# Optimization experiments

Hardware: AMD Instinct MI355X
Metric: run time of the kernel (lower is better)

The kernel has to match this reference:

```python
import jax, jax.numpy as jnp
import numpy as np

B, S, D = 2, 2048, 2048
H, DH = 16, 128


def _rope(x, position):
    # x: [B, H, S, DH], position: [B, S]
    dh = x.shape[-1]
    inv_freq = 1.0 / (10000.0 ** (jnp.arange(0, dh, 2, dtype=jnp.float32) / dh))
    freqs = position.astype(jnp.float32)[:, :, None] * inv_freq[None, None, :]  # [B, S, DH/2]
    emb = jnp.concatenate([freqs, freqs], axis=-1)  # [B, S, DH]
    cos = jnp.cos(emb)[:, None, :, :]
    sin = jnp.sin(emb)[:, None, :, :]
    x1, x2 = x[..., : dh // 2], x[..., dh // 2 :]
    rot = jnp.concatenate([-x2, x1], axis=-1)
    return x * cos + rot * sin


def setup_inputs() -> dict:
    key = jax.random.key(0)
    ks = jax.random.split(key, 5)
    hidden_state = jax.random.normal(ks[0], (B, S, D), dtype=jnp.float32)
    mask = jnp.broadcast_to(jnp.tril(jnp.ones((S, S), dtype=bool)), (B, S, S))
    position = jnp.broadcast_to(jnp.arange(S, dtype=jnp.int64), (B, S))
    scale = 1.0 / np.sqrt(D)
    Wq = jax.random.normal(ks[1], (D, H * DH), dtype=jnp.float32) * scale
    Wk = jax.random.normal(ks[2], (D, H * DH), dtype=jnp.float32) * scale
    Wv = jax.random.normal(ks[3], (D, H * DH), dtype=jnp.float32) * scale
    Wo = jax.random.normal(ks[4], (H * DH, D), dtype=jnp.float32) * scale
    return {"hidden_state": hidden_state, "mask": mask, "position": position,
            "Wq": Wq, "Wk": Wk, "Wv": Wv, "Wo": Wo}


def reference(hidden_state, mask, position, Wq, Wk, Wv, Wo):
    b, s, _ = hidden_state.shape
    def split_heads(h):
        return h.reshape(b, s, H, DH).transpose(0, 2, 1, 3)  # [B, H, S, DH]
    h_q = _rope(split_heads(hidden_state @ Wq), position)
    h_k = _rope(split_heads(hidden_state @ Wk), position)
    h_v = split_heads(hidden_state @ Wv)
    score = jnp.einsum('bhqd,bhkd->bhqk', h_q, h_k) / np.sqrt(DH)
    m = mask[:, None, :, :]
    score = jnp.where(m, score, jnp.float32(-jnp.inf))
    probs = jax.nn.softmax(score, axis=-1)
    probs = jnp.where(m, probs, jnp.float32(0.0))
    out = jnp.einsum('bhqk,bhkd->bhqd', probs, h_v)
    out = out.transpose(0, 2, 1, 3).reshape(b, s, H * DH)
    return out @ Wo
```

## Files before the change

### kernel.cpp

```cpp
#include <hip/hip_runtime.h>
#include <hip/hip_bf16.h>

typedef unsigned short u16;
typedef __bf16 bf16x8 __attribute__((ext_vector_type(8)));
typedef float f32x4 __attribute__((ext_vector_type(4)));
typedef unsigned short u16x8 __attribute__((ext_vector_type(8)));

__device__ __forceinline__ u16 f2bf(float f) {
  union { float f; unsigned u; } v; v.f = f;
  unsigned r = (v.u + 0x7FFFu + ((v.u >> 16) & 1u)) >> 16;
  return (u16)r;
}
__device__ __forceinline__ float bf2f(u16 s) {
  union { unsigned u; float f; } v; v.u = ((unsigned)s) << 16;
  return v.f;
}
__device__ __forceinline__ f32x4 zero4() { f32x4 z = {0.f, 0.f, 0.f, 0.f}; return z; }

__device__ __forceinline__ void async16(void* lds, const void* g) {
  __builtin_amdgcn_global_load_lds(
      (__attribute__((address_space(1))) void*)(void*)g,
      (__attribute__((address_space(3))) void*)lds, 16, 0, 0);
}

__global__ void sniff_dtype(const unsigned* __restrict__ X, int* __restrict__ flag) {
  __shared__ int cnt;
  if (threadIdx.x == 0) cnt = 0;
  __syncthreads();
  unsigned w = X[(size_t)threadIdx.x * 16384 + 1000];
  int e = (int)((w >> 7) & 0xFF);
  if (e >= 100 && e <= 150) atomicAdd(&cnt, 1);
  __syncthreads();
  if (threadIdx.x == 0) flag[0] = (cnt < 192) ? 1 : 0;
}

__global__ __launch_bounds__(256) void convert_x(
    const void* __restrict__ X, u16* __restrict__ dst, const int* __restrict__ flag) {
  const int mode = flag[0];
  size_t i8 = ((size_t)blockIdx.x * 256 + threadIdx.x) * 8;
  if (mode) {
    const float4* f = (const float4*)X;
    float4 a = f[i8 / 4], b = f[i8 / 4 + 1];
    u16x8 o;
    o[0] = f2bf(a.x); o[1] = f2bf(a.y); o[2] = f2bf(a.z); o[3] = f2bf(a.w);
    o[4] = f2bf(b.x); o[5] = f2bf(b.y); o[6] = f2bf(b.z); o[7] = f2bf(b.w);
    *(u16x8*)&dst[i8] = o;
  } else {
    *(u16x8*)&dst[i8] = *(const u16x8*)&((const u16*)X)[i8];
  }
}

__global__ __launch_bounds__(256) void transpose_w(
    const void* __restrict__ src, u16* __restrict__ d, const int* __restrict__ flag)
{
  __shared__ u16 t[64][65];
  const int mode = flag[0];
  int r0 = blockIdx.y * 64, c0 = blockIdx.x * 64;
  int tid = threadIdx.x;
  for (int j = 0; j < 2; ++j) {
    int idx = tid + j * 256;
    int r = idx >> 3, c = (idx & 7) * 8;
    size_t base = (size_t)(r0 + r) * 2048 + c0 + c;
    if (mode) {
      const float4* f = (const float4*)src;
      float4 a = f[base / 4], b = f[base / 4 + 1];
      t[r][c + 0] = f2bf(a.x); t[r][c + 1] = f2bf(a.y);
      t[r][c + 2] = f2bf(a.z); t[r][c + 3] = f2bf(a.w);
      t[r][c + 4] = f2bf(b.x); t[r][c + 5] = f2bf(b.y);
      t[r][c + 6] = f2bf(b.z); t[r][c + 7] = f2bf(b.w);
    } else {
      u16x8 v = *(const u16x8*)&((const u16*)src)[base];
      for (int q = 0; q < 8; ++q) t[r][c + q] = v[q];
    }
  }
  __syncthreads();
  for (int j = 0; j < 2; ++j) {
    int idx = tid + j * 256;
    int c = idx >> 3, r = (idx & 7) * 8;
    u16x8 v;
    for (int q = 0; q < 8; ++q) v[q] = t[r + q][c];
    *(u16x8*)&d[(size_t)(c0 + c) * 2048 + r0 + r] = v;
  }
}

__global__ __launch_bounds__(256) void transpose_v(
    const u16* __restrict__ V, u16* __restrict__ Vt)
{
  __shared__ u16 t[64][65];
  int bh = blockIdx.z;
  int b = bh >> 4, h = bh & 15;
  int kv0 = blockIdx.x * 64, d0 = blockIdx.y * 64;
  int tid = threadIdx.x;
  for (int j = 0; j < 2; ++j) {
    int idx = tid + j * 256;
    int r = idx >> 3, c = (idx & 7) * 8;
    u16x8 v = *(const u16x8*)&V[(size_t)(b * 2048 + kv0 + r) * 2048 + h * 128 + d0 + c];
    for (int q = 0; q < 8; ++q) t[r][c + q] = v[q];
  }
  __syncthreads();
  for (int j = 0; j < 2; ++j) {
    int idx = tid + j * 256;
    int c = idx >> 3, r = (idx & 7) * 8;
    u16x8 v;
    for (int q = 0; q < 8; ++q) v[q] = t[r + q][c];
    *(u16x8*)&Vt[((size_t)bh * 128 + d0 + c) * 2048 + kv0 + r] = v;
  }
}

__global__ __launch_bounds__(256) void rope_k(u16* __restrict__ Qp, u16* __restrict__ Kp)
{
  int idx = blockIdx.x * 256 + threadIdx.x;
  u16* X = blockIdx.y ? Kp : Qp;
  int i8 = (idx & 7) * 8;
  int h = (idx >> 3) & 15;
  int tok = idx >> 7;
  int pos = tok & 2047;
  size_t base = (size_t)tok * 2048 + h * 128 + i8;
  u16x8 a = *(const u16x8*)&X[base];
  u16x8 bv = *(const u16x8*)&X[base + 64];
  u16x8 ra, rb;
  for (int j = 0; j < 8; ++j) {
    float fi = (float)(i8 + j);
    float invf = __expf(fi * -0.14391156831212787f);
    float th = (float)pos * invf;
    float c, s;
    sincosf(th, &s, &c);
    float x1 = bf2f(a[j]), x2 = bf2f(bv[j]);
    ra[j] = f2bf(x1 * c - x2 * s);
    rb[j] = f2bf(x2 * c + x1 * s);
  }
  *(u16x8*)&X[base] = ra;
  *(u16x8*)&X[base + 64] = rb;
}

__global__ __launch_bounds__(256) void qkv_gemm(
    const u16* __restrict__ A, const u16* __restrict__ Bt,
    u16* __restrict__ Qw, u16* __restrict__ Kw, u16* __restrict__ Vw)
{
  __shared__ __align__(16) u16 As[128 * 32];
  __shared__ __align__(16) u16 Bs[128 * 32];
  const int K = 2048, N = 2048;
  const int tid = threadIdx.x;
  const int wave = tid >> 6, lane = tid & 63;
  const int quad = lane >> 4, l = lane & 15;
  const int wr = wave >> 1, wc = wave & 1;
  const int m0 = blockIdx.y * 128, n0full = blockIdx.x * 128;
  const int mat = n0full >> 11;
  const int n0 = n0full & 2047;
  u16* C = (mat == 0) ? Qw : ((mat == 1) ? Kw : Vw);

  f32x4 acc[4][4];
  for (int i = 0; i < 4; ++i)
    for (int j = 0; j < 4; ++j) acc[i][j] = zero4();

  int rowA[2], gA[2];
  for (int j = 0; j < 2; ++j) {
    int tf = tid + j * 256;
    rowA[j] = tf >> 2;
    gA[j] = (tf & 3) ^ ((rowA[j] >> 1) & 3);
  }

  for (int kt = 0; kt < K; kt += 32) {
    __syncthreads();
    for (int j = 0; j < 2; ++j) {
      int tf = tid + j * 256;
      async16(&As[tf * 8], &A[(size_t)(m0 + rowA[j]) * K + kt + gA[j] * 8]);
      async16(&Bs[tf * 8], &Bt[(size_t)(n0full + rowA[j]) * K + kt + gA[j] * 8]);
    }
    __syncthreads();

    bf16x8 af[4], bfr[4];
    for (int mt = 0; mt < 4; ++mt) {
      int row = wr * 64 + mt * 16 + l;
      int g = quad ^ ((row >> 1) & 3);
      af[mt] = *(const bf16x8*)&As[row * 32 + g * 8];
    }
    for (int nt = 0; nt < 4; ++nt) {
      int row = wc * 64 + nt * 16 + l;
      int g = quad ^ ((row >> 1) & 3);
      bfr[nt] = *(const bf16x8*)&Bs[row * 32 + g * 8];
    }
    for (int mt = 0; mt < 4; ++mt)
      for (int nt = 0; nt < 4; ++nt)
        acc[mt][nt] = __builtin_amdgcn_mfma_f32_16x16x32_bf16(af[mt], bfr[nt], acc[mt][nt], 0, 0, 0);
  }
  for (int mt = 0; mt < 4; ++mt)
    for (int nt = 0; nt < 4; ++nt)
      for (int r = 0; r < 4; ++r) {
        int m = m0 + wr * 64 + mt * 16 + quad * 4 + r;
        int n = n0 + wc * 64 + nt * 16 + l;
        C[(size_t)m * N + n] = f2bf(acc[mt][nt][r]);
      }
}

__global__ __launch_bounds__(256) void gemm64_bt(
    const u16* __restrict__ A, const u16* __restrict__ Bt, void* __restrict__ C,
    int M, int N, int K, const int* __restrict__ flag, int dual)
{
  __shared__ __align__(16) u16 As[64 * 32];
  __shared__ __align__(16) u16 Bs[64 * 32];
  const int mode = dual ? flag[0] : 0;
  const int tid = threadIdx.x;
  const int wave = tid >> 6, lane = tid & 63;
  const int quad = lane >> 4, l = lane & 15;
  const int wr = wave >> 1, wc = wave & 1;
  const int m0 = blockIdx.y * 64, n0 = blockIdx.x * 64;

  f32x4 acc[2][2];
  for (int i = 0; i < 2; ++i)
    for (int j = 0; j < 2; ++j) acc[i][j] = zero4();

  const int rowA = tid >> 2;
  const int gA = (tid & 3) ^ ((rowA >> 1) & 3);

  for (int kt = 0; kt < K; kt += 32) {
    __syncthreads();
    async16(&As[tid * 8], &A[(size_t)(m0 + rowA) * K + kt + gA * 8]);
    async16(&Bs[tid * 8], &Bt[(size_t)(n0 + rowA) * K + kt + gA * 8]);
    __syncthreads();

    bf16x8 af[2], bfr[2];
    for (int mt = 0; mt < 2; ++mt) {
      int row = wr * 32 + mt * 16 + l;
      int g = quad ^ ((row >> 1) & 3);
      af[mt] = *(const bf16x8*)&As[row * 32 + g * 8];
    }
    for (int nt = 0; nt < 2; ++nt) {
      int row = wc * 32 + nt * 16 + l;
      int g = quad ^ ((row >> 1) & 3);
      bfr[nt] = *(const bf16x8*)&Bs[row * 32 + g * 8];
    }
    for (int mt = 0; mt < 2; ++mt)
      for (int nt = 0; nt < 2; ++nt)
        acc[mt][nt] = __builtin_amdgcn_mfma_f32_16x16x32_bf16(af[mt], bfr[nt], acc[mt][nt], 0, 0, 0);
  }
  for (int mt = 0; mt < 2; ++mt)
    for (int nt = 0; nt < 2; ++nt)
      for (int r = 0; r < 4; ++r) {
        int m = m0 + wr * 32 + mt * 16 + quad * 4 + r;
        int n = n0 + wc * 32 + nt * 16 + l;
        if (mode) ((float*)C)[(size_t)m * N + n] = acc[mt][nt][r];
        else      ((u16*)C)[(size_t)m * N + n] = f2bf(acc[mt][nt][r]);
      }
}

__global__ __launch_bounds__(256) void flash_k(
    const u16* __restrict__ Q, const u16* __restrict__ K,
    const u16* __restrict__ Vt, u16* __restrict__ O)
{
  __shared__ __align__(16) u16 Ks[64 * 128];
  __shared__ __align__(16) u16 Vs[128 * 64];
  __shared__ __align__(16) u16 Ps[4][16 * 64];

  const int tid = threadIdx.x;
  const int wave = tid >> 6, lane = tid & 63;
  const int quad = lane >> 4, l = lane & 15;
  const int pair = blockIdx.x;
  const int h = blockIdx.y, b = blockIdx.z;

  const size_t kbase = ((size_t)b * 2048) * 2048 + h * 128;
  const size_t vbase = ((size_t)(b * 16 + h)) * 128 * 2048;

  for (int half = 0; half < 2; ++half) {
    const int qt = half ? pair : (31 - pair);

    const size_t qoff = ((size_t)(b * 2048 + qt * 64)) * 2048 + h * 128;
    bf16x8 qf[4];
    for (int ks = 0; ks < 4; ++ks)
      qf[ks] = *(const bf16x8*)&Q[qoff + (size_t)(wave * 16 + l) * 2048 + (ks * 4 + quad) * 8];

    f32x4 Oacc[8];
    for (int i = 0; i < 8; ++i) Oacc[i] = zero4();
    float mi[4] = {-3e38f, -3e38f, -3e38f, -3e38f};
    float li[4] = {0.f, 0.f, 0.f, 0.f};

    for (int kt = 0; kt <= qt; ++kt) {
      __syncthreads();
      for (int j = 0; j < 4; ++j) {
        int tf = tid + j * 256;
        int row = tf >> 4, p = tf & 15;
        int g = p ^ (row & 7);
        async16(&Ks[tf * 8], &K[kbase + (size_t)(kt * 64 + row) * 2048 + g * 8]);
      }
      for (int j = 0; j < 4; ++j) {
        int tf = tid + j * 256;
        int row = tf >> 3, p = tf & 7;
        int g = p ^ (row & 7);
        async16(&Vs[tf * 8], &Vt[vbase + (size_t)row * 2048 + kt * 64 + g * 8]);
      }
      __syncthreads();

      f32x4 S[4];
      for (int nt = 0; nt < 4; ++nt) S[nt] = zero4();
      for (int ks = 0; ks < 4; ++ks) {
        int g = ks * 4 + quad;
        for (int nt = 0; nt < 4; ++nt) {
          bf16x8 bk = *(const bf16x8*)&Ks[(nt * 16 + l) * 128 + (g ^ (l & 7)) * 8];
          S[nt] = __builtin_amdgcn_mfma_f32_16x16x32_bf16(qf[ks], bk, S[nt], 0, 0, 0);
        }
      }

      const bool dg = (kt == qt);
      float Pv[4][4];
      float rm[4] = {-3e38f, -3e38f, -3e38f, -3e38f};
      for (int nt = 0; nt < 4; ++nt)
        for (int r = 0; r < 4; ++r) {
          float s = S[nt][r] * 0.08838834764831845f;
          if (dg && (nt * 16 + l > wave * 16 + quad * 4 + r)) s = -3e38f;
          Pv[nt][r] = s;
          rm[r] = fmaxf(rm[r], s);
        }
      for (int r = 0; r < 4; ++r)
        for (int off = 1; off < 16; off <<= 1)
          rm[r] = fmaxf(rm[r], __shfl_xor(rm[r], off));
      float al[4], rs[4];
      for (int r = 0; r < 4; ++r) {
        float mn = fmaxf(mi[r], rm[r]);
        al[r] = __expf(mi[r] - mn);
        mi[r] = mn;
        rs[r] = 0.f;
      }
      for (int nt = 0; nt < 4; ++nt)
        for (int r = 0; r < 4; ++r) {
          float p = __expf(Pv[nt][r] - mi[r]);
          Pv[nt][r] = p;
          rs[r] += p;
        }
      for (int r = 0; r < 4; ++r) {
        for (int off = 1; off < 16; off <<= 1)
          rs[r] += __shfl_xor(rs[r], off);
        li[r] = li[r] * al[r] + rs[r];
      }
      for (int nt = 0; nt < 4; ++nt) {
        int gc = nt * 2 + (l >> 3);
        for (int r = 0; r < 4; ++r) {
          int row = quad * 4 + r;
          Ps[wave][row * 64 + ((gc ^ (row & 7)) * 8) + (l & 7)] = f2bf(Pv[nt][r]);
        }
      }
      for (int d = 0; d < 8; ++d)
        for (int r = 0; r < 4; ++r) Oacc[d][r] *= al[r];
      for (int ks = 0; ks < 2; ++ks) {
        int g = ks * 4 + quad;
        bf16x8 ap = *(const bf16x8*)&Ps[wave][l * 64 + (g ^ (l & 7)) * 8];
        for (int d = 0; d < 8; ++d) {
          bf16x8 bv = *(const bf16x8*)&Vs[(d * 16 + l) * 64 + (g ^ (l & 7)) * 8];
          Oacc[d] = __builtin_amdgcn_mfma_f32_16x16x32_bf16(ap, bv, Oacc[d], 0, 0, 0);
        }
      }
    }

    float inv[4];
    for (int r = 0; r < 4; ++r) inv[r] = 1.f / li[r];
    size_t obase = ((size_t)(b * 2048 + qt * 64 + wave * 16)) * 2048 + h * 128;
    for (int d = 0; d < 8; ++d)
      for (int r = 0; r < 4; ++r)
        O[obase + (size_t)(quad * 4 + r) * 2048 + d * 16 + l] = f2bf(Oacc[d][r] * inv[r]);
  }
}

extern "C" void kernel_launch(void* const* d_in, const int* in_sizes, int n_in,
                              void* d_out, int out_size, void* d_ws, size_t ws_size,
                              hipStream_t stream) {
  const void* X  = d_in[0];
  const void* Wq = d_in[3];
  const void* Wk = d_in[4];
  const void* Wv = d_in[5];
  const void* Wo = d_in[6];

  u16* base = (u16*)d_ws;
  int* flag = (int*)d_ws;
  const size_t TOK = 4096, DM = 2048;
  u16* Xbf = base + 128;
  u16* Qw  = Xbf + TOK * DM;
  u16* Kw  = Qw + TOK * DM;
  u16* Vw  = Kw + TOK * DM;
  u16* WT3 = Vw + TOK * DM;
  u16* Vtw = Xbf;

  sniff_dtype<<<1, 256, 0, stream>>>((const unsigned*)X, flag);
  convert_x<<<4096, 256, 0, stream>>>(X, Xbf, flag);

  transpose_w<<<dim3(32, 32), 256, 0, stream>>>(Wq, WT3, flag);
  transpose_w<<<dim3(32, 32), 256, 0, stream>>>(Wk, WT3 + DM * DM, flag);
  transpose_w<<<dim3(32, 32), 256, 0, stream>>>(Wv, WT3 + 2 * DM * DM, flag);
  qkv_gemm<<<dim3(48, 32), 256, 0, stream>>>(Xbf, WT3, Qw, Kw, Vw);

  rope_k<<<dim3(2048, 2), 256, 0, stream>>>(Qw, Kw);
  transpose_v<<<dim3(32, 2, 32), 256, 0, stream>>>(Vw, Vtw);
  flash_k<<<dim3(16, 16, 2), 256, 0, stream>>>(Qw, Kw, Vtw, Vw);

  transpose_w<<<dim3(32, 32), 256, 0, stream>>>(Wo, WT3, flag);
  gemm64_bt<<<dim3(32, 64), 256, 0, stream>>>(Vw, WT3, d_out, 4096, 2048, 2048, flag, 1);
}
```

Baseline: 499.9 us.

## Double-buffer LDS tiles in QKV GEMM, output GEMM and flash attention

Adds a second LDS buffer to the QKV GEMM, the 64x64 GEMM and the flash attention kernel. The async global-to-LDS load of the next K/V or A/B tile is issued before the MFMA work on the current tile. This aims to hide global load latency behind compute and removes one barrier per step. In exchange it doubles tile LDS usage: the flash kernel rises to about 72KB, which may lower occupancy. It also relies on the barrier waiting for the outstanding async loads.

```diff
diff --git a/kernel.cpp b/kernel.cpp
--- a/kernel.cpp
+++ b/kernel.cpp
@@ -133,12 +133,45 @@
   *(u16x8*)&X[base + 64] = rb;
 }
 
+__device__ __forceinline__ void qkv_stage(
+    u16* As, u16* Bs, const u16* A, const u16* Bt,
+    int m0, int n0full, int kt, int tid, const int* rowA, const int* gA)
+{
+  for (int j = 0; j < 2; ++j) {
+    int tf = tid + j * 256;
+    async16(&As[tf * 8], &A[(size_t)(m0 + rowA[j]) * 2048 + kt + gA[j] * 8]);
+    async16(&Bs[tf * 8], &Bt[(size_t)(n0full + rowA[j]) * 2048 + kt + gA[j] * 8]);
+  }
+}
+
+__device__ __forceinline__ void qkv_compute(
+    const u16* As, const u16* Bs, f32x4 (&acc)[4][4],
+    int wr, int wc, int quad, int l)
+{
+  bf16x8 af[4], bfr[4];
+  for (int mt = 0; mt < 4; ++mt) {
+    int row = wr * 64 + mt * 16 + l;
+    int g = quad ^ ((row >> 1) & 3);
+    af[mt] = *(const bf16x8*)&As[row * 32 + g * 8];
+  }
+  for (int nt = 0; nt < 4; ++nt) {
+    int row = wc * 64 + nt * 16 + l;
+    int g = quad ^ ((row >> 1) & 3);
+    bfr[nt] = *(const bf16x8*)&Bs[row * 32 + g * 8];
+  }
+  for (int mt = 0; mt < 4; ++mt)
+    for (int nt = 0; nt < 4; ++nt)
+      acc[mt][nt] = __builtin_amdgcn_mfma_f32_16x16x32_bf16(af[mt], bfr[nt], acc[mt][nt], 0, 0, 0);
+}
+
 __global__ __launch_bounds__(256) void qkv_gemm(
     const u16* __restrict__ A, const u16* __restrict__ Bt,
     u16* __restrict__ Qw, u16* __restrict__ Kw, u16* __restrict__ Vw)
 {
-  __shared__ __align__(16) u16 As[128 * 32];
-  __shared__ __align__(16) u16 Bs[128 * 32];
+  __shared__ __align__(16) u16 As0[128 * 32];
+  __shared__ __align__(16) u16 Bs0[128 * 32];
+  __shared__ __align__(16) u16 As1[128 * 32];
+  __shared__ __align__(16) u16 Bs1[128 * 32];
   const int K = 2048, N = 2048;
   const int tid = threadIdx.x;
   const int wave = tid >> 6, lane = tid & 63;
@@ -160,30 +193,19 @@
     gA[j] = (tf & 3) ^ ((rowA[j] >> 1) & 3);
   }
 
-  for (int kt = 0; kt < K; kt += 32) {
+  qkv_stage(As0, Bs0, A, Bt, m0, n0full, 0, tid, rowA, gA);
+  __syncthreads();
+
+  for (int kt = 0; kt < K; kt += 64) {
+    qkv_stage(As1, Bs1, A, Bt, m0, n0full, kt + 32, tid, rowA, gA);
+    qkv_compute(As0, Bs0, acc, wr, wc, quad, l);
     __syncthreads();
-    for (int j = 0; j < 2; ++j) {
-      int tf = tid + j * 256;
-      async16(&As[tf * 8], &A[(size_t)(m0 + rowA[j]) * K + kt + gA[j] * 8]);
-      async16(&Bs[tf * 8], &Bt[(size_t)(n0full + rowA[j]) * K + kt + gA[j] * 8]);
-    }
+    if (kt + 64 < K)
+      qkv_stage(As0, Bs0, A, Bt, m0, n0full, kt + 64, tid, rowA, gA);
+    qkv_compute(As1, Bs1, acc, wr, wc, quad, l);
     __syncthreads();
-
-    bf16x8 af[4], bfr[4];
-    for (int mt = 0; mt < 4; ++mt) {
-      int row = wr * 64 + mt * 16 + l;
-      int g = quad ^ ((row >> 1) & 3);
-      af[mt] = *(const bf16x8*)&As[row * 32 + g * 8];
-    }
-    for (int nt = 0; nt < 4; ++nt) {
-      int row = wc * 64 + nt * 16 + l;
-      int g = quad ^ ((row >> 1) & 3);
-      bfr[nt] = *(const bf16x8*)&Bs[row * 32 + g * 8];
-    }
-    for (int mt = 0; mt < 4; ++mt)
-      for (int nt = 0; nt < 4; ++nt)
-        acc[mt][nt] = __builtin_amdgcn_mfma_f32_16x16x32_bf16(af[mt], bfr[nt], acc[mt][nt], 0, 0, 0);
-  }
+  }
+
   for (int mt = 0; mt < 4; ++mt)
     for (int nt = 0; nt < 4; ++nt)
       for (int r = 0; r < 4; ++r) {
@@ -193,12 +215,34 @@
       }
 }
 
+__device__ __forceinline__ void g64_compute(
+    const u16* As, const u16* Bs, f32x4 (&acc)[2][2],
+    int wr, int wc, int quad, int l)
+{
+  bf16x8 af[2], bfr[2];
+  for (int mt = 0; mt < 2; ++mt) {
+    int row = wr * 32 + mt * 16 + l;
+    int g = quad ^ ((row >> 1) & 3);
+    af[mt] = *(const bf16x8*)&As[row * 32 + g * 8];
+  }
+  for (int nt = 0; nt < 2; ++nt) {
+    int row = wc * 32 + nt * 16 + l;
+    int g = quad ^ ((row >> 1) & 3);
+    bfr[nt] = *(const bf16x8*)&Bs[row * 32 + g * 8];
+  }
+  for (int mt = 0; mt < 2; ++mt)
+    for (int nt = 0; nt < 2; ++nt)
+      acc[mt][nt] = __builtin_amdgcn_mfma_f32_16x16x32_bf16(af[mt], bfr[nt], acc[mt][nt], 0, 0, 0);
+}
+
 __global__ __launch_bounds__(256) void gemm64_bt(
     const u16* __restrict__ A, const u16* __restrict__ Bt, void* __restrict__ C,
     int M, int N, int K, const int* __restrict__ flag, int dual)
 {
-  __shared__ __align__(16) u16 As[64 * 32];
-  __shared__ __align__(16) u16 Bs[64 * 32];
+  __shared__ __align__(16) u16 As0[64 * 32];
+  __shared__ __align__(16) u16 Bs0[64 * 32];
+  __shared__ __align__(16) u16 As1[64 * 32];
+  __shared__ __align__(16) u16 Bs1[64 * 32];
   const int mode = dual ? flag[0] : 0;
   const int tid = threadIdx.x;
   const int wave = tid >> 6, lane = tid & 63;
@@ -213,27 +257,23 @@
   const int rowA = tid >> 2;
   const int gA = (tid & 3) ^ ((rowA >> 1) & 3);
 
-  for (int kt = 0; kt < K; kt += 32) {
+  async16(&As0[tid * 8], &A[(size_t)(m0 + rowA) * K + gA * 8]);
+  async16(&Bs0[tid * 8], &Bt[(size_t)(n0 + rowA) * K + gA * 8]);
+  __syncthreads();
+
+  for (int kt = 0; kt < K; kt += 64) {
+    async16(&As1[tid * 8], &A[(size_t)(m0 + rowA) * K + kt + 32 + gA * 8]);
+    async16(&Bs1[tid * 8], &Bt[(size_t)(n0 + rowA) * K + kt + 32 + gA * 8]);
+    g64_compute(As0, Bs0, acc, wr, wc, quad, l);
     __syncthreads();
-    async16(&As[tid * 8], &A[(size_t)(m0 + rowA) * K + kt + gA * 8]);
-    async16(&Bs[tid * 8], &Bt[(size_t)(n0 + rowA) * K + kt + gA * 8]);
+    if (kt + 64 < K) {
+      async16(&As0[tid * 8], &A[(size_t)(m0 + rowA) * K + kt + 64 + gA * 8]);
+      async16(&Bs0[tid * 8], &Bt[(size_t)(n0 + rowA) * K + kt + 64 + gA * 8]);
+    }
+    g64_compute(As1, Bs1, acc, wr, wc, quad, l);
     __syncthreads();
-
-    bf16x8 af[2], bfr[2];
-    for (int mt = 0; mt < 2; ++mt) {
-      int row = wr * 32 + mt * 16 + l;
-      int g = quad ^ ((row >> 1) & 3);
-      af[mt] = *(const bf16x8*)&As[row * 32 + g * 8];
-    }
-    for (int nt = 0; nt < 2; ++nt) {
-      int row = wc * 32 + nt * 16 + l;
-      int g = quad ^ ((row >> 1) & 3);
-      bfr[nt] = *(const bf16x8*)&Bs[row * 32 + g * 8];
-    }
-    for (int mt = 0; mt < 2; ++mt)
-      for (int nt = 0; nt < 2; ++nt)
-        acc[mt][nt] = __builtin_amdgcn_mfma_f32_16x16x32_bf16(af[mt], bfr[nt], acc[mt][nt], 0, 0, 0);
-  }
+  }
+
   for (int mt = 0; mt < 2; ++mt)
     for (int nt = 0; nt < 2; ++nt)
       for (int r = 0; r < 4; ++r) {
@@ -244,12 +284,32 @@
       }
 }
 
+__device__ __forceinline__ void fl_stage(
+    u16* Ks, u16* Vs, const u16* K, const u16* Vt,
+    size_t kbase, size_t vbase, int kt, int tid)
+{
+  for (int j = 0; j < 4; ++j) {
+    int tf = tid + j * 256;
+    int row = tf >> 4, p = tf & 15;
+    int g = p ^ (row & 7);
+    async16(&Ks[tf * 8], &K[kbase + (size_t)(kt * 64 + row) * 2048 + g * 8]);
+  }
+  for (int j = 0; j < 4; ++j) {
+    int tf = tid + j * 256;
+    int row = tf >> 3, p = tf & 7;
+    int g = p ^ (row & 7);
+    async16(&Vs[tf * 8], &Vt[vbase + (size_t)row * 2048 + kt * 64 + g * 8]);
+  }
+}
+
 __global__ __launch_bounds__(256) void flash_k(
     const u16* __restrict__ Q, const u16* __restrict__ K,
     const u16* __restrict__ Vt, u16* __restrict__ O)
 {
-  __shared__ __align__(16) u16 Ks[64 * 128];
-  __shared__ __align__(16) u16 Vs[128 * 64];
+  __shared__ __align__(16) u16 Ks0[64 * 128];
+  __shared__ __align__(16) u16 Vs0[128 * 64];
+  __shared__ __align__(16) u16 Ks1[64 * 128];
+  __shared__ __align__(16) u16 Vs1[128 * 64];
   __shared__ __align__(16) u16 Ps[4][16 * 64];
 
   const int tid = threadIdx.x;
@@ -274,28 +334,13 @@
     float mi[4] = {-3e38f, -3e38f, -3e38f, -3e38f};
     float li[4] = {0.f, 0.f, 0.f, 0.f};
 
-    for (int kt = 0; kt <= qt; ++kt) {
-      __syncthreads();
-      for (int j = 0; j < 4; ++j) {
-        int tf = tid + j * 256;
-        int row = tf >> 4, p = tf & 15;
-        int g = p ^ (row & 7);
-        async16(&Ks[tf * 8], &K[kbase + (size_t)(kt * 64 + row) * 2048 + g * 8]);
-      }
-      for (int j = 0; j < 4; ++j) {
-        int tf = tid + j * 256;
-        int row = tf >> 3, p = tf & 7;
-        int g = p ^ (row & 7);
-        async16(&Vs[tf * 8], &Vt[vbase + (size_t)row * 2048 + kt * 64 + g * 8]);
-      }
-      __syncthreads();
-
+    auto fl_body = [&](const u16* Ksb, const u16* Vsb, int kt) {
       f32x4 S[4];
       for (int nt = 0; nt < 4; ++nt) S[nt] = zero4();
       for (int ks = 0; ks < 4; ++ks) {
         int g = ks * 4 + quad;
         for (int nt = 0; nt < 4; ++nt) {
-          bf16x8 bk = *(const bf16x8*)&Ks[(nt * 16 + l) * 128 + (g ^ (l & 7)) * 8];
+          bf16x8 bk = *(const bf16x8*)&Ksb[(nt * 16 + l) * 128 + (g ^ (l & 7)) * 8];
           S[nt] = __builtin_amdgcn_mfma_f32_16x16x32_bf16(qf[ks], bk, S[nt], 0, 0, 0);
         }
       }
@@ -344,9 +389,23 @@
         int g = ks * 4 + quad;
         bf16x8 ap = *(const bf16x8*)&Ps[wave][l * 64 + (g ^ (l & 7)) * 8];
         for (int d = 0; d < 8; ++d) {
-          bf16x8 bv = *(const bf16x8*)&Vs[(d * 16 + l) * 64 + (g ^ (l & 7)) * 8];
+          bf16x8 bv = *(const bf16x8*)&Vsb[(d * 16 + l) * 64 + (g ^ (l & 7)) * 8];
           Oacc[d] = __builtin_amdgcn_mfma_f32_16x16x32_bf16(ap, bv, Oacc[d], 0, 0, 0);
         }
+      }
+    };
+
+    fl_stage(Ks0, Vs0, K, Vt, kbase, vbase, 0, tid);
+    __syncthreads();
+
+    for (int kt = 0; kt <= qt; kt += 2) {
+      if (kt + 1 <= qt) fl_stage(Ks1, Vs1, K, Vt, kbase, vbase, kt + 1, tid);
+      fl_body(Ks0, Vs0, kt);
+      __syncthreads();
+      if (kt + 1 <= qt) {
+        if (kt + 2 <= qt) fl_stage(Ks0, Vs0, K, Vt, kbase, vbase, kt + 2, tid);
+        fl_body(Ks1, Vs1, kt + 1);
+        __syncthreads();
       }
     }
 
```

New measurement: 482.9 us. -3.4%, faster.
